# Performance work log

Measured on AMD Instinct MI355X. Metric: run time of the kernel, lower is better.

Reference implementation:

```python
import jax, jax.numpy as jnp
import numpy as np

HAD_G = 32  # hadamard_group_size == MX block size (scales are [out, in//32])

# FP4 E2M1 magnitude grid and decision midpoints (round-to-nearest)
_FP4_LEVELS = jnp.array([0.0, 0.5, 1.0, 1.5, 2.0, 3.0, 4.0, 6.0], dtype=jnp.float32)
_FP4_MIDS = jnp.array([0.25, 0.75, 1.25, 1.75, 2.5, 3.5, 5.0], dtype=jnp.float32)


def _hadamard(n: int) -> np.ndarray:
    H = np.array([[1.0]], dtype=np.float32)
    while H.shape[0] < n:
        H = np.block([[H, H], [H, -H]])
    return H * (n ** -0.5)


def mxfp4_quant_dequant(v):
    """MXFP4 quantize-dequantize along the last axis (block of 32).
    v: [..., 32]. Shared power-of-2 scale per block (E8M0, absmax-based),
    elements rounded to nearest FP4 (E2M1) value. Straight-through estimator.
    """
    amax = jnp.max(jnp.abs(v), axis=-1, keepdims=True)
    # scale = 2^(floor(log2(amax)) - emax_fp4), emax_fp4 = 2 (6 = 1.5 * 2^2)
    e = jnp.floor(jnp.log2(jnp.maximum(amax, jnp.float32(1e-30)))) - 2.0
    scale = jnp.exp2(e)
    a = v / scale
    mag = jnp.minimum(jnp.abs(a), 6.0)
    q = _FP4_LEVELS[jnp.digitize(mag, _FP4_MIDS)] * jnp.sign(a)
    deq = q * scale
    # STE: identity gradient through the quantizer (matches custom autograd Fn)
    return v + jax.lax.stop_gradient(deq - v)


def _rotate_quant(t, H):
    """Per-group Hadamard rotation then MXFP4 quant-dequant. t: [N, K]."""
    N, K = t.shape
    tg = t.reshape(N, K // HAD_G, HAD_G)
    tr = jnp.einsum('ngh,hk->ngk', tg, H)  # rotate each 32-group
    return mxfp4_quant_dequant(tr).reshape(N, K)


def setup_inputs() -> dict:
    key = jax.random.key(0)
    kx, kw, kb = jax.random.split(key, 3)
    B, S, K, O = 4, 2048, 4096, 16384
    x = jax.random.normal(kx, (B, S, K), dtype=jnp.float32)
    weight = jax.random.normal(kw, (O, K), dtype=jnp.float32) * 0.02
    bias = jax.random.normal(kb, (O,), dtype=jnp.float32) * 0.01
    fwd_hadamard = jnp.asarray(_hadamard(HAD_G))
    return {"x": x, "weight": weight, "bias": bias, "fwd_hadamard": fwd_hadamard}


def reference(x, weight, bias, fwd_hadamard):
    B, S, K = x.shape
    O = weight.shape[0]
    xq = _rotate_quant(x.reshape(B * S, K), fwd_hadamard)   # deq(q(x H))
    wq = _rotate_quant(weight, fwd_hadamard)                # deq(q(W H))
    # H H^T = I, so (xH)(WH)^T approximates x W^T; GEMM runs on quantized values
    y = xq @ wq.T + bias
    return y.reshape(B, S, O)
```

## Files before the change

### kernel.cpp

```cpp
#include <hip/hip_runtime.h>

typedef unsigned short u16;
typedef unsigned int u32;
typedef unsigned char u8;
typedef int v8i __attribute__((ext_vector_type(8)));
typedef int v4i __attribute__((ext_vector_type(4)));
typedef int v2i __attribute__((ext_vector_type(2)));
typedef float v16f __attribute__((ext_vector_type(16)));

#define INV_SQRT32 0.17677669529663688f

#define QOFS_OUT 32768
#define QOFS_SC  36864

__global__ __launch_bounds__(256) void rotquant4_kernel(
    const float* __restrict__ T, u8* __restrict__ Q4, u8* __restrict__ S,
    int K, int ntk, int nkb )
{
    __shared__ __align__(16) u8 smem[37120];

    const int tid  = threadIdx.x;
    const int bid  = blockIdx.x;
    const int rblk = bid / nkb;
    const int kblk = bid - rblk * nkb;
    const int row0 = rblk * 8;
    const int kb0  = kblk * 32;
    const int t0g  = (row0 >> 7) * ntk + (kb0 >> 2);
    const int rl   = row0 & 127;

    {
        const float4* src = (const float4*)T;
#pragma unroll
        for (int j = 0; j < 8; ++j) {
            float4 t = src[(size_t)(row0 + j) * (K >> 2) + (kblk << 8) + tid];
            int kb = tid >> 3, i = tid & 7;
            *(float4*)(smem + j * 4096 + kb * 128 + ((i ^ (kb & 7)) << 4)) = t;
        }
    }
    __syncthreads();

    {
        const int rr = tid >> 5;
        const int kb = tid & 31;

        float v[32];
#pragma unroll
        for (int i = 0; i < 8; ++i) {
            float4 t = *(const float4*)(smem + rr * 4096 + kb * 128
                                        + ((i ^ (kb & 7)) << 4));
            v[i*4+0] = t.x; v[i*4+1] = t.y; v[i*4+2] = t.z; v[i*4+3] = t.w;
        }

#pragma unroll
        for (int s = 1; s < 32; s <<= 1) {
#pragma unroll
            for (int i = 0; i < 32; ++i) {
                if (!(i & s)) {
                    float a = v[i], b = v[i | s];
                    v[i] = a + b;
                    v[i | s] = a - b;
                }
            }
        }

        float amax = 0.f;
#pragma unroll
        for (int i = 0; i < 32; ++i) {
            v[i] *= INV_SQRT32;
            amax = fmaxf(amax, fabsf(v[i]));
        }

        u32 ab = __float_as_uint(amax);
        int be = (int)(ab >> 23);
        u32 w[4] = {0u, 0u, 0u, 0u};
        u8 sbyte = 0;
        if (be >= 3) {
            sbyte = (u8)(be - 2);
            float iscale = __uint_as_float((u32)(256 - be) << 23);
#pragma unroll
            for (int i = 0; i < 32; ++i) {
                float a = v[i] * iscale;
                float m = fminf(fabsf(a), 6.0f);
                int c = (m < 0.25f) ? 0 :
                        (m < 0.75f) ? 1 :
                        (m < 1.25f) ? 2 :
                        (m < 1.75f) ? 3 :
                        (m < 2.5f)  ? 4 :
                        (m < 3.5f)  ? 5 :
                        (m < 5.0f)  ? 6 : 7;
                c |= (int)((__float_as_uint(a) >> 28) & 8u);
                w[i >> 3] |= (u32)c << (4 * (i & 7));
            }
        }

        uint4 p; p.x = w[0]; p.y = w[1]; p.z = w[2]; p.w = w[3];
        *(uint4*)(smem + QOFS_OUT + rr * 512 + (kb >> 2) * 64 + (kb & 3) * 16) = p;
        smem[QOFS_SC + rr * 32 + (kb >> 2) * 4 + (kb & 3)] = sbyte;
    }
    __syncthreads();

    {
        int tileL = tid >> 5, slot = (tid >> 3) & 3, rr = tid & 7;
        uint4 p = *(const uint4*)(smem + QOFS_OUT + rr * 512 + tileL * 64
                                  + slot * 16);
        ((uint4*)Q4)[(size_t)(t0g + tileL) * 512 + slot * 128 + rl + rr] = p;
    }
    if (tid < 64) {
        int tileL = tid >> 3, rr = tid & 7;
        u32 sc = *(const u32*)(smem + QOFS_SC + rr * 32 + tileL * 4);
        int r7 = rl + rr;
        ((u32*)S)[(size_t)(t0g + tileL) * 128 + ((r7 & 31) << 2)
                  + ((r7 >> 5) & 3)] = sc;
    }
}

__device__ __forceinline__ void gload16(const void* g, void* l)
{
    __builtin_amdgcn_global_load_lds(
        (__attribute__((address_space(1))) void*)g,
        (__attribute__((address_space(3))) void*)l, 16, 0, 0);
}
__device__ __forceinline__ void gload4(const void* g, void* l)
{
    __builtin_amdgcn_global_load_lds(
        (__attribute__((address_space(1))) void*)g,
        (__attribute__((address_space(3))) void*)l, 4, 0, 0);
}

#define BUF_BYTES 34816
#define OFS_B     16384
#define OFS_AS    32768
#define OFS_BS    33792
#define BB0 0
#define BB1 BUF_BYTES
#define BB2 (2 * BUF_BYTES)

__global__ __launch_bounds__(512, 2) void gemm4_bias(
    const u8* __restrict__ A4, const u8* __restrict__ AS,
    const u8* __restrict__ B4, const u8* __restrict__ BS,
    const float* __restrict__ bias, float* __restrict__ C,
    int M, int N, int K)
{
    __shared__ __align__(16) u8 smem[3 * BUF_BYTES];

    const int tid  = threadIdx.x;
    const int wave = tid >> 6;
    const int lane = tid & 63;
    const int l31  = lane & 31;
    const int lhi  = lane >> 5;
    const int wm   = wave >> 2;
    const int wn   = wave & 3;
    const int ntk  = K >> 7;
    const int NT   = ntk;

    const int nbn = N >> 8;
    const int nbm = M >> 8;
    int bid = blockIdx.x;
    int bm, bn;
    if (((gridDim.x & 7) == 0) && ((nbm & 7) == 0)) {
        int bpc = nbm >> 3;
        int lb  = __builtin_ctz(bpc);
        int c   = bid & 7;
        int r   = bid >> 3;
        bm = c * bpc + (r & (bpc - 1));
        bn = r >> lb;
    } else {
        bn = bid % nbn;
        bm = bid / nbn;
    }

    v16f acc[4][2];
#pragma unroll
    for (int i = 0; i < 4; ++i)
#pragma unroll
        for (int j = 0; j < 2; ++j)
#pragma unroll
            for (int r = 0; r < 16; ++r) acc[i][j][r] = 0.f;

    const size_t aRow0 = (size_t)(2 * bm) * ntk;
    const size_t bRow0 = (size_t)(2 * bn) * ntk;
    const int isA = (wave < 4);
    const int w4  = wave & 3;
    const u8* scB = isA ? AS : BS;
    const size_t scT = (size_t)((isA ? 2 * bm : 2 * bn) + (w4 >> 1)) * ntk;
    const int scInner = (w4 & 1) * 256 + lane * 4;
    const int scDst   = (isA ? OFS_AS : OFS_BS) + w4 * 256;
    const int gOfs = wave * 1024 + lane * 16;
    const int lOfs = wave * 1024;

    const int aRB = wm * 8192 + lhi * 2048 + l31 * 16;
    const int bRB = OFS_B + (wn >> 1) * 8192 + lhi * 2048
                    + (wn & 1) * 1024 + l31 * 16;
    const int asB = OFS_AS + wm * 512 + l31 * 16;
    const int bsB = OFS_BS + (wn >> 1) * 512 + (wn & 1) * 8 + l31 * 16;
    const int sh0 = lhi * 8;
    const int sh1 = sh0 + 16;

#define STG_A(bofs, kt, r)                                                    \
    gload16(A4 + ((aRow0 + (size_t)(r) * ntk + (kt)) << 13) + gOfs,           \
            smem + (bofs) + (r) * 8192 + lOfs)
#define STG_B(bofs, kt, r)                                                    \
    gload16(B4 + ((bRow0 + (size_t)(r) * ntk + (kt)) << 13) + gOfs,           \
            smem + (bofs) + OFS_B + (r) * 8192 + lOfs)
#define STG_S(bofs, kt)                                                       \
    gload4(scB + ((scT + (kt)) << 9) + scInner, smem + (bofs) + scDst)
#define STAGE(bofs, kt)                                                       \
    do { STG_A(bofs, kt, 0); STG_A(bofs, kt, 1);                              \
         STG_B(bofs, kt, 0); STG_B(bofs, kt, 1); STG_S(bofs, kt); } while (0)

#define MK8(x) __builtin_shufflevector(x, x, 0, 1, 2, 3, -1, -1, -1, -1)
#define MFMA1(mi, ni, AF, BF, SA, SB)                                         \
    acc[mi][ni] = __builtin_amdgcn_mfma_scale_f32_32x32x64_f8f6f4(            \
        MK8(AF), MK8(BF), acc[mi][ni], 4, 4, 0, (int)(SA), 0, (int)(SB))

#define TILE(CO, NO, PO, kt, ST, REFILL, FINAL)                               \
    do {                                                                      \
        if (ST) STAGE(PO, (kt) + 2);                                          \
                       \
        u32 ya0 = ((u32)SAv[0] >> sh0) & 0xffu;                               \
        u32 ya1 = ((u32)SAv[1] >> sh0) & 0xffu;                               \
        u32 ya2 = ((u32)SAv[2] >> sh0) & 0xffu;                               \
        u32 ya3 = ((u32)SAv[3] >> sh0) & 0xffu;                               \
        u32 yb0 = ((u32)SBv[0] >> sh0) & 0xffu;                               \
        u32 yb1 = ((u32)SBv[1] >> sh0) & 0xffu;                               \
        u32 xa0 = ((u32)SAv[0] >> sh1) & 0xffu;                               \
        u32 xa1 = ((u32)SAv[1] >> sh1) & 0xffu;                               \
        u32 xa2 = ((u32)SAv[2] >> sh1) & 0xffu;                               \
        u32 xa3 = ((u32)SAv[3] >> sh1) & 0xffu;                               \
        u32 xb0 = ((u32)SBv[0] >> sh1) & 0xffu;                               \
        u32 xb1 = ((u32)SBv[1] >> sh1) & 0xffu;                               \
        __builtin_amdgcn_s_setprio(1);                                        \
        v4i a2 = *(const v4i*)(smem + (CO) + aRB + 1024);                     \
        v4i a3 = *(const v4i*)(smem + (CO) + aRB + 1536);                     \
        MFMA1(0, 0, A0a, B0a, ya0, yb0); MFMA1(0, 1, A0a, B0b, ya0, yb1);     \
        v4i b1a = *(const v4i*)(smem + (CO) + bRB + 4096);                    \
        v4i b1b = *(const v4i*)(smem + (CO) + bRB + 4608);                    \
        MFMA1(1, 0, A0b, B0a, ya1, yb0); MFMA1(1, 1, A0b, B0b, ya1, yb1);     \
        v4i a10 = *(const v4i*)(smem + (CO) + aRB + 4096);                    \
        v4i a11 = *(const v4i*)(smem + (CO) + aRB + 4608);                    \
        MFMA1(2, 0, a2, B0a, ya2, yb0); MFMA1(2, 1, a2, B0b, ya2, yb1);       \
        v4i a12 = *(const v4i*)(smem + (CO) + aRB + 5120);                    \
        v4i a13 = *(const v4i*)(smem + (CO) + aRB + 5632);                    \
        MFMA1(3, 0, a3, B0a, ya3, yb0); MFMA1(3, 1, a3, B0b, ya3, yb1);       \
        __builtin_amdgcn_s_setprio(0);                                        \
        if (!(FINAL)) {                                                       \
            if (ST) { asm volatile("s_waitcnt vmcnt(5)" ::: "memory"); }      \
            else    { asm volatile("s_waitcnt vmcnt(0)" ::: "memory"); }      \
            __builtin_amdgcn_s_barrier();                                     \
        }                                                                     \
        __builtin_amdgcn_s_setprio(1);                                        \
        if (REFILL) { SAv = *(const v4i*)(smem + (NO) + asB);                 \
                      SBv = *(const v2i*)(smem + (NO) + bsB); }               \
        MFMA1(0, 0, a10, b1a, xa0, xb0); MFMA1(0, 1, a10, b1b, xa0, xb1);     \
        if (REFILL) { B0a = *(const v4i*)(smem + (NO) + bRB);                 \
                      B0b = *(const v4i*)(smem + (NO) + bRB + 512); }         \
        MFMA1(1, 0, a11, b1a, xa1, xb0); MFMA1(1, 1, a11, b1b, xa1, xb1);     \
        if (REFILL) { A0a = *(const v4i*)(smem + (NO) + aRB);                 \
                      A0b = *(const v4i*)(smem + (NO) + aRB + 512); }         \
        MFMA1(2, 0, a12, b1a, xa2, xb0); MFMA1(2, 1, a12, b1b, xa2, xb1);     \
        MFMA1(3, 0, a13, b1a, xa3, xb0); MFMA1(3, 1, a13, b1b, xa3, xb1);     \
        __builtin_amdgcn_s_setprio(0);                                        \
    } while (0)

    STAGE(BB0, 0);
    STAGE(BB1, 1);
    asm volatile("s_waitcnt vmcnt(5)" ::: "memory");
    __builtin_amdgcn_s_barrier();

    v4i SAv = *(const v4i*)(smem + BB0 + asB);
    v2i SBv = *(const v2i*)(smem + BB0 + bsB);
    v4i B0a = *(const v4i*)(smem + BB0 + bRB);
    v4i B0b = *(const v4i*)(smem + BB0 + bRB + 512);
    v4i A0a = *(const v4i*)(smem + BB0 + aRB);
    v4i A0b = *(const v4i*)(smem + BB0 + aRB + 512);

#pragma unroll 1
    for (int t = 0; t + 2 < NT; t += 3) {
        TILE(BB0, BB1, BB2, t + 0, true, true, false);
        TILE(BB1, BB2, BB0, t + 1, true, true, false);
        TILE(BB2, BB0, BB1, t + 2, true, true, false);
    }
    TILE(BB0, BB1, BB2, NT - 2, false, true, false);
    TILE(BB1, BB2, BB0, NT - 1, false, false, true);

    const int cb = bn * 256 + wn * 64;
    const int rb = bm * 256 + wm * 128;
#pragma unroll
    for (int ni = 0; ni < 2; ++ni) {
        float bb = bias[cb + ni * 32 + l31];
#pragma unroll
        for (int mi = 0; mi < 4; ++mi) {
#pragma unroll
            for (int reg = 0; reg < 16; ++reg) {
                int row = (reg & 3) + 8 * (reg >> 2) + 4 * lhi;
                C[(size_t)(rb + mi * 32 + row) * N + cb + ni * 32 + l31]
                    = acc[mi][ni][reg] + bb;
            }
        }
    }
#undef STG_A
#undef STG_B
#undef STG_S
#undef STAGE
#undef MK8
#undef MFMA1
#undef TILE
}

extern "C" void kernel_launch(void* const* d_in, const int* in_sizes, int n_in,
                              void* d_out, int out_size, void* d_ws, size_t ws_size,
                              hipStream_t stream)
{
    const float* x    = (const float*)d_in[0];
    const float* w    = (const float*)d_in[1];
    const float* bias = (const float*)d_in[2];

    const int O = in_sizes[2];
    const int K = in_sizes[1] / O;
    const int M = in_sizes[0] / K;

    u8* x4 = (u8*)d_ws;
    u8* w4 = x4 + (size_t)M * (K / 2);
    u8* xs = w4 + (size_t)O * (K / 2);
    u8* ws = xs + (size_t)M * (K / 32);

    const int ntk = K / 128;
    const int nkb = K / 1024;
    rotquant4_kernel<<<(M / 8) * nkb, 256, 0, stream>>>(x, x4, xs, K, ntk, nkb);
    rotquant4_kernel<<<(O / 8) * nkb, 256, 0, stream>>>(w, w4, ws, K, ntk, nkb);

    dim3 grid((M / 256) * (O / 256));
    gemm4_bias<<<grid, 512, 0, stream>>>(x4, xs, w4, ws, bias, (float*)d_out,
                                         M, O, K);
}
```

Baseline: 441.3 us.

## Load B tiles directly into registers instead of staging through LDS

B operand tiles and their scales are now read from global memory straight into per-wave registers, double-buffered one k-step ahead, while only A and its scales stay staged through LDS. This halves the LDS buffer size and removes the LDS write/read traffic for B. In exchange, each wave pair reads B redundantly from global/L2, register pressure goes up, and the vmcnt accounting changes. The loop is unrolled by six, with tail handling that assumes NT is a specific multiple.

```diff
diff --git a/kernel.cpp b/kernel.cpp
--- a/kernel.cpp
+++ b/kernel.cpp
@@ -5,7 +5,6 @@
 typedef unsigned char u8;
 typedef int v8i __attribute__((ext_vector_type(8)));
 typedef int v4i __attribute__((ext_vector_type(4)));
-typedef int v2i __attribute__((ext_vector_type(2)));
 typedef float v16f __attribute__((ext_vector_type(16)));
 
 #define INV_SQRT32 0.17677669529663688f
@@ -127,10 +126,8 @@
         (__attribute__((address_space(3))) void*)l, 4, 0, 0);
 }
 
-#define BUF_BYTES 34816
-#define OFS_B     16384
-#define OFS_AS    32768
-#define OFS_BS    33792
+#define BUF_BYTES 17408
+#define OFS_AS    16384
 #define BB0 0
 #define BB1 BUF_BYTES
 #define BB2 (2 * BUF_BYTES)
@@ -178,110 +175,121 @@
             for (int r = 0; r < 16; ++r) acc[i][j][r] = 0.f;
 
     const size_t aRow0 = (size_t)(2 * bm) * ntk;
-    const size_t bRow0 = (size_t)(2 * bn) * ntk;
-    const int isA = (wave < 4);
-    const int w4  = wave & 3;
-    const u8* scB = isA ? AS : BS;
-    const size_t scT = (size_t)((isA ? 2 * bm : 2 * bn) + (w4 >> 1)) * ntk;
-    const int scInner = (w4 & 1) * 256 + lane * 4;
-    const int scDst   = (isA ? OFS_AS : OFS_BS) + w4 * 256;
+    const int w4   = wave & 3;
+    const size_t ascT = (size_t)(2 * bm + (w4 >> 1)) * ntk;
+    const int ascOfs  = (w4 & 1) * 256 + lane * 4;
     const int gOfs = wave * 1024 + lane * 16;
     const int lOfs = wave * 1024;
 
+    const size_t bTileRow = (size_t)(2 * bn + (wn >> 1)) * ntk;
+    const int bInner   = lhi * 2048 + ((wn & 1) * 64 + l31) * 16;
+    const int bScInner = l31 * 4 + (wn & 1) * 2;
+
     const int aRB = wm * 8192 + lhi * 2048 + l31 * 16;
-    const int bRB = OFS_B + (wn >> 1) * 8192 + lhi * 2048
-                    + (wn & 1) * 1024 + l31 * 16;
     const int asB = OFS_AS + wm * 512 + l31 * 16;
-    const int bsB = OFS_BS + (wn >> 1) * 512 + (wn & 1) * 8 + l31 * 16;
     const int sh0 = lhi * 8;
     const int sh1 = sh0 + 16;
 
 #define STG_A(bofs, kt, r)                                                    \
     gload16(A4 + ((aRow0 + (size_t)(r) * ntk + (kt)) << 13) + gOfs,           \
             smem + (bofs) + (r) * 8192 + lOfs)
-#define STG_B(bofs, kt, r)                                                    \
-    gload16(B4 + ((bRow0 + (size_t)(r) * ntk + (kt)) << 13) + gOfs,           \
-            smem + (bofs) + OFS_B + (r) * 8192 + lOfs)
-#define STG_S(bofs, kt)                                                       \
-    gload4(scB + ((scT + (kt)) << 9) + scInner, smem + (bofs) + scDst)
+#define STG_AS(bofs, kt)                                                      \
+    gload4(AS + ((ascT + (kt)) << 9) + ascOfs,                                \
+           smem + (bofs) + OFS_AS + w4 * 256)
 #define STAGE(bofs, kt)                                                       \
-    do { STG_A(bofs, kt, 0); STG_A(bofs, kt, 1);                              \
-         STG_B(bofs, kt, 0); STG_B(bofs, kt, 1); STG_S(bofs, kt); } while (0)
+    do { STG_A(bofs, kt, 0); STG_A(bofs, kt, 1); STG_AS(bofs, kt); } while (0)
+
+#define LOADB(B0, B1, B2, B3, SB0, SB1, kt)                                   \
+    do {                                                                      \
+        const u8* bb_ = B4 + ((bTileRow + (size_t)(kt)) << 13) + bInner;      \
+        B0 = *(const v4i*)(bb_);                                              \
+        B1 = *(const v4i*)(bb_ + 512);                                        \
+        B2 = *(const v4i*)(bb_ + 4096);                                       \
+        B3 = *(const v4i*)(bb_ + 4608);                                       \
+        const u32* bs_ = (const u32*)(BS + ((bTileRow + (size_t)(kt)) << 9))  \
+                         + bScInner;                                          \
+        SB0 = bs_[0]; SB1 = bs_[1];                                           \
+    } while (0)
 
 #define MK8(x) __builtin_shufflevector(x, x, 0, 1, 2, 3, -1, -1, -1, -1)
 #define MFMA1(mi, ni, AF, BF, SA, SB)                                         \
     acc[mi][ni] = __builtin_amdgcn_mfma_scale_f32_32x32x64_f8f6f4(            \
         MK8(AF), MK8(BF), acc[mi][ni], 4, 4, 0, (int)(SA), 0, (int)(SB))
 
-#define TILE(CO, NO, PO, kt, ST, REFILL, FINAL)                               \
+#define TILE(CO, NO, PO, kt, BC0, BC1, BC2, BC3, SBC0, SBC1,                  \
+             BN0_, BN1_, BN2_, BN3_, SBN0_, SBN1_, LDB, ST, REFILL, FINAL, VMN)\
     do {                                                                      \
+        if (LDB) LOADB(BN0_, BN1_, BN2_, BN3_, SBN0_, SBN1_, (kt) + 1);       \
         if (ST) STAGE(PO, (kt) + 2);                                          \
-                       \
         u32 ya0 = ((u32)SAv[0] >> sh0) & 0xffu;                               \
         u32 ya1 = ((u32)SAv[1] >> sh0) & 0xffu;                               \
         u32 ya2 = ((u32)SAv[2] >> sh0) & 0xffu;                               \
         u32 ya3 = ((u32)SAv[3] >> sh0) & 0xffu;                               \
-        u32 yb0 = ((u32)SBv[0] >> sh0) & 0xffu;                               \
-        u32 yb1 = ((u32)SBv[1] >> sh0) & 0xffu;                               \
         u32 xa0 = ((u32)SAv[0] >> sh1) & 0xffu;                               \
         u32 xa1 = ((u32)SAv[1] >> sh1) & 0xffu;                               \
         u32 xa2 = ((u32)SAv[2] >> sh1) & 0xffu;                               \
         u32 xa3 = ((u32)SAv[3] >> sh1) & 0xffu;                               \
-        u32 xb0 = ((u32)SBv[0] >> sh1) & 0xffu;                               \
-        u32 xb1 = ((u32)SBv[1] >> sh1) & 0xffu;                               \
+        u32 yb0 = (SBC0 >> sh0) & 0xffu, yb1 = (SBC1 >> sh0) & 0xffu;         \
+        u32 xb0 = (SBC0 >> sh1) & 0xffu, xb1 = (SBC1 >> sh1) & 0xffu;         \
         __builtin_amdgcn_s_setprio(1);                                        \
         v4i a2 = *(const v4i*)(smem + (CO) + aRB + 1024);                     \
         v4i a3 = *(const v4i*)(smem + (CO) + aRB + 1536);                     \
-        MFMA1(0, 0, A0a, B0a, ya0, yb0); MFMA1(0, 1, A0a, B0b, ya0, yb1);     \
-        v4i b1a = *(const v4i*)(smem + (CO) + bRB + 4096);                    \
-        v4i b1b = *(const v4i*)(smem + (CO) + bRB + 4608);                    \
-        MFMA1(1, 0, A0b, B0a, ya1, yb0); MFMA1(1, 1, A0b, B0b, ya1, yb1);     \
+        MFMA1(0, 0, A0a, BC0, ya0, yb0); MFMA1(0, 1, A0a, BC1, ya0, yb1);     \
         v4i a10 = *(const v4i*)(smem + (CO) + aRB + 4096);                    \
         v4i a11 = *(const v4i*)(smem + (CO) + aRB + 4608);                    \
-        MFMA1(2, 0, a2, B0a, ya2, yb0); MFMA1(2, 1, a2, B0b, ya2, yb1);       \
+        MFMA1(1, 0, A0b, BC0, ya1, yb0); MFMA1(1, 1, A0b, BC1, ya1, yb1);     \
         v4i a12 = *(const v4i*)(smem + (CO) + aRB + 5120);                    \
         v4i a13 = *(const v4i*)(smem + (CO) + aRB + 5632);                    \
-        MFMA1(3, 0, a3, B0a, ya3, yb0); MFMA1(3, 1, a3, B0b, ya3, yb1);       \
+        MFMA1(2, 0, a2, BC0, ya2, yb0); MFMA1(2, 1, a2, BC1, ya2, yb1);       \
+        MFMA1(3, 0, a3, BC0, ya3, yb0); MFMA1(3, 1, a3, BC1, ya3, yb1);       \
         __builtin_amdgcn_s_setprio(0);                                        \
         if (!(FINAL)) {                                                       \
-            if (ST) { asm volatile("s_waitcnt vmcnt(5)" ::: "memory"); }      \
-            else    { asm volatile("s_waitcnt vmcnt(0)" ::: "memory"); }      \
+            asm volatile("s_waitcnt vmcnt(%0)" :: "i"(VMN) : "memory");       \
             __builtin_amdgcn_s_barrier();                                     \
         }                                                                     \
         __builtin_amdgcn_s_setprio(1);                                        \
         if (REFILL) { SAv = *(const v4i*)(smem + (NO) + asB);                 \
-                      SBv = *(const v2i*)(smem + (NO) + bsB); }               \
-        MFMA1(0, 0, a10, b1a, xa0, xb0); MFMA1(0, 1, a10, b1b, xa0, xb1);     \
-        if (REFILL) { B0a = *(const v4i*)(smem + (NO) + bRB);                 \
-                      B0b = *(const v4i*)(smem + (NO) + bRB + 512); }         \
-        MFMA1(1, 0, a11, b1a, xa1, xb0); MFMA1(1, 1, a11, b1b, xa1, xb1);     \
-        if (REFILL) { A0a = *(const v4i*)(smem + (NO) + aRB);                 \
+                      A0a = *(const v4i*)(smem + (NO) + aRB);                 \
                       A0b = *(const v4i*)(smem + (NO) + aRB + 512); }         \
-        MFMA1(2, 0, a12, b1a, xa2, xb0); MFMA1(2, 1, a12, b1b, xa2, xb1);     \
-        MFMA1(3, 0, a13, b1a, xa3, xb0); MFMA1(3, 1, a13, b1b, xa3, xb1);     \
+        MFMA1(0, 0, a10, BC2, xa0, xb0); MFMA1(0, 1, a10, BC3, xa0, xb1);     \
+        MFMA1(1, 0, a11, BC2, xa1, xb0); MFMA1(1, 1, a11, BC3, xa1, xb1);     \
+        MFMA1(2, 0, a12, BC2, xa2, xb0); MFMA1(2, 1, a12, BC3, xa2, xb1);     \
+        MFMA1(3, 0, a13, BC2, xa3, xb0); MFMA1(3, 1, a13, BC3, xa3, xb1);     \
         __builtin_amdgcn_s_setprio(0);                                        \
     } while (0)
 
+    v4i bP0, bP1, bP2, bP3, bQ0, bQ1, bQ2, bQ3;
+    u32 sbP0, sbP1, sbQ0, sbQ1;
+
+    LOADB(bP0, bP1, bP2, bP3, sbP0, sbP1, 0);
     STAGE(BB0, 0);
     STAGE(BB1, 1);
-    asm volatile("s_waitcnt vmcnt(5)" ::: "memory");
+    asm volatile("s_waitcnt vmcnt(3)" ::: "memory");
     __builtin_amdgcn_s_barrier();
 
     v4i SAv = *(const v4i*)(smem + BB0 + asB);
-    v2i SBv = *(const v2i*)(smem + BB0 + bsB);
-    v4i B0a = *(const v4i*)(smem + BB0 + bRB);
-    v4i B0b = *(const v4i*)(smem + BB0 + bRB + 512);
     v4i A0a = *(const v4i*)(smem + BB0 + aRB);
     v4i A0b = *(const v4i*)(smem + BB0 + aRB + 512);
 
 #pragma unroll 1
-    for (int t = 0; t + 2 < NT; t += 3) {
-        TILE(BB0, BB1, BB2, t + 0, true, true, false);
-        TILE(BB1, BB2, BB0, t + 1, true, true, false);
-        TILE(BB2, BB0, BB1, t + 2, true, true, false);
-    }
-    TILE(BB0, BB1, BB2, NT - 2, false, true, false);
-    TILE(BB1, BB2, BB0, NT - 1, false, false, true);
+    for (int t = 0; t + 7 < NT; t += 6) {
+        TILE(BB0, BB1, BB2, t + 0, bP0, bP1, bP2, bP3, sbP0, sbP1,
+             bQ0, bQ1, bQ2, bQ3, sbQ0, sbQ1, true, true, true, false, 9);
+        TILE(BB1, BB2, BB0, t + 1, bQ0, bQ1, bQ2, bQ3, sbQ0, sbQ1,
+             bP0, bP1, bP2, bP3, sbP0, sbP1, true, true, true, false, 9);
+        TILE(BB2, BB0, BB1, t + 2, bP0, bP1, bP2, bP3, sbP0, sbP1,
+             bQ0, bQ1, bQ2, bQ3, sbQ0, sbQ1, true, true, true, false, 9);
+        TILE(BB0, BB1, BB2, t + 3, bQ0, bQ1, bQ2, bQ3, sbQ0, sbQ1,
+             bP0, bP1, bP2, bP3, sbP0, sbP1, true, true, true, false, 9);
+        TILE(BB1, BB2, BB0, t + 4, bP0, bP1, bP2, bP3, sbP0, sbP1,
+             bQ0, bQ1, bQ2, bQ3, sbQ0, sbQ1, true, true, true, false, 9);
+        TILE(BB2, BB0, BB1, t + 5, bQ0, bQ1, bQ2, bQ3, sbQ0, sbQ1,
+             bP0, bP1, bP2, bP3, sbP0, sbP1, true, true, true, false, 9);
+    }
+    TILE(BB0, BB1, BB2, NT - 2, bP0, bP1, bP2, bP3, sbP0, sbP1,
+         bQ0, bQ1, bQ2, bQ3, sbQ0, sbQ1, true, false, true, false, 6);
+    TILE(BB1, BB2, BB0, NT - 1, bQ0, bQ1, bQ2, bQ3, sbQ0, sbQ1,
+         bP0, bP1, bP2, bP3, sbP0, sbP1, false, false, false, true, 0);
 
     const int cb = bn * 256 + wn * 64;
     const int rb = bm * 256 + wm * 128;
@@ -299,9 +307,9 @@
         }
     }
 #undef STG_A
-#undef STG_B
-#undef STG_S
+#undef STG_AS
 #undef STAGE
+#undef LOADB
 #undef MK8
 #undef MFMA1
 #undef TILE
```

After: 501.8 us. +13.7%, slower.
